# Optimization experiments

Measured on AMD Instinct MI355X. Metric: run time of the kernel, lower is better.

The kernel has to match this reference:

```python
import jax, jax.numpy as jnp
import numpy as np

N_NODES = 50000
N_EDGES = 600000
C = 128
T = 2          # layer index t
NU = 1         # DRew nu parameter
EPS = 0.0      # GIN eps


def mlp(x, W1, b1, W2, b2):
    # instantiate_mlp with final_activation=False, batch_norm=False:
    # Linear -> ReLU -> Linear
    return jax.nn.relu(x @ W1 + b1) @ W2 + b2


def setup_inputs() -> dict:
    key = jax.random.key(0)
    ks = jax.random.split(key, 16)
    node_embeddings = jax.random.normal(ks[0], (T + 1, N_NODES, C), dtype=jnp.float32)
    edge_index = jax.random.randint(ks[1], (2, N_EDGES), 0, N_NODES, dtype=jnp.int32)
    edge_weights = jax.random.randint(ks[2], (N_EDGES,), 1, T + 2, dtype=jnp.int32)  # hops 1..3
    s = 1.0 / np.sqrt(C)
    def lin(k):
        kw, kb = jax.random.split(k)
        return (jax.random.uniform(kw, (C, C), jnp.float32, -s, s),
                jax.random.uniform(kb, (C,), jnp.float32, -s, s))
    loop_W1, loop_b1 = lin(ks[3]); loop_W2, loop_b2 = lin(ks[4])
    rel_W1, rel_b1 = lin(ks[5]); rel_W2, rel_b2 = lin(ks[6])
    # T higher-hop MLPs (k = 2 .. T+1), stacked along axis 0
    hh1 = [lin(k) for k in jax.random.split(ks[7], T)]
    hh2 = [lin(k) for k in jax.random.split(ks[8], T)]
    hh_W1 = jnp.stack([w for w, _ in hh1]); hh_b1 = jnp.stack([b for _, b in hh1])
    hh_W2 = jnp.stack([w for w, _ in hh2]); hh_b2 = jnp.stack([b for _, b in hh2])
    hop_coef = jax.random.normal(ks[9], (T + 1,), dtype=jnp.float32)
    return dict(t=T, node_embeddings=node_embeddings, edge_index=edge_index,
                edge_weights=edge_weights,
                loop_W1=loop_W1, loop_b1=loop_b1, loop_W2=loop_W2, loop_b2=loop_b2,
                rel_W1=rel_W1, rel_b1=rel_b1, rel_W2=rel_W2, rel_b2=rel_b2,
                hh_W1=hh_W1, hh_b1=hh_b1, hh_W2=hh_W2, hh_b2=hh_b2,
                hop_coef=hop_coef)


def reference(t, node_embeddings, edge_index, edge_weights,
              loop_W1, loop_b1, loop_W2, loop_b2,
              rel_W1, rel_b1, rel_W2, rel_b2,
              hh_W1, hh_b1, hh_W2, hh_b2, hop_coef):
    x_t = node_embeddings[t]                       # [N, C]
    n = x_t.shape[0]
    row, col = edge_index[0], edge_index[1]        # sparse A: out[row] += X[col]
    dt = x_t.dtype

    hops = []
    # hop 1: relational MLP on current-layer embeddings
    h1 = mlp(x_t, rel_W1, rel_b1, rel_W2, rel_b2)
    m1 = (edge_weights == 1).astype(dt)[:, None]
    hops.append(jax.ops.segment_sum(h1[col] * m1, row, num_segments=n))
    # hops k = 2 .. t+1: per-hop MLP on delayed embeddings (DRew)
    for k in range(2, t + 2):
        delay = max(0, k - NU)
        hk = mlp(node_embeddings[t - delay],
                 hh_W1[k - 2], hh_b1[k - 2], hh_W2[k - 2], hh_b2[k - 2])
        mk = (edge_weights == k).astype(dt)[:, None]
        hops.append(jax.ops.segment_sum(hk[col] * mk, row, num_segments=n))

    by_hop = jnp.stack(hops)                       # [t+1, N, C]
    self_term = mlp((1.0 + EPS) * x_t, loop_W1, loop_b1, loop_W2, loop_b2)
    return self_term + jnp.einsum('k,knc->nc', hop_coef, by_hop)
```

## Files before the change

### kernel.cpp

```cpp
#include <hip/hip_runtime.h>

#define N_NODES 50000
#define N_EDGES 600000
#define C 128
#define STRIPS 3125
#define GROUPS 3125
#define N_TASKS 4

typedef __bf16 bf16;
typedef __attribute__((ext_vector_type(8))) __bf16 bf16x8;
typedef __attribute__((ext_vector_type(4))) __bf16 bf16x4;
typedef __attribute__((ext_vector_type(2))) __bf16 bf16x2;
typedef __attribute__((ext_vector_type(4))) float f32x4;
typedef __attribute__((ext_vector_type(2))) float f32x2;

struct PtrsV { const void* p[8]; };

__device__ __forceinline__ int bf16_wild(unsigned short w) {
    int exp = (w >> 7) & 0xFF;
    int mant = w & 0x7F;
    if (exp == 0xFF) return 1;
    if (exp >= 133) return 1;
    if (exp == 0) return mant != 0 ? 1 : 0;
    if (exp <= 114) return 1;
    return 0;
}

__global__ void __launch_bounds__(256) detect_zero_kernel(
    const unsigned short* __restrict__ emb,
    const unsigned short* __restrict__ w,
    const unsigned short* __restrict__ b,
    const unsigned short* __restrict__ hc,
    int* __restrict__ flags, int* __restrict__ deg)
{
    if (blockIdx.x == 0) {
        int lane = threadIdx.x;
        if (lane >= 64) return;
        int ce = 0, cw = 0, cb = 0, ch = 0;
        for (int j = 0; j < 4; ++j) {
            ce += bf16_wild(emb[lane * 4 + j]);
            cw += bf16_wild(w[lane * 4 + j]);
        }
        for (int j = 0; j < 2; ++j) cb += bf16_wild(b[lane * 2 + j]);
        if (lane < 3) ch = bf16_wild(hc[lane]);
        for (int off = 32; off > 0; off >>= 1) {
            ce += __shfl_down(ce, off);
            cw += __shfl_down(cw, off);
            cb += __shfl_down(cb, off);
            ch += __shfl_down(ch, off);
        }
        if (lane == 0) {
            int wf = (cw >= 16) ? 1 : 0;
            flags[0] = (ce >= 16) ? 1 : 0;
            flags[1] = wf;
            flags[2] = (cb >= 8) ? 1 : 0;
            flags[3] = (ch > 0) ? 1 : wf;
        }
    } else {
        int i = (blockIdx.x - 1) * 256 + threadIdx.x;
        if (i < N_NODES) deg[i] = 0;
    }
}

__global__ void __launch_bounds__(256) pack_kernel(
    PtrsV wmats, PtrsV bvecs, const void* hc_raw,
    const int* __restrict__ flags,
    bf16* __restrict__ pw, float* __restrict__ cbias, float* __restrict__ ccoef)
{
    int tid = blockIdx.x * 256 + threadIdx.x;
    int wf = flags[1], bfl = flags[2], hf = flags[3];
    if (tid < 8 * 16384) {
        int m    = tid >> 14;
        int r    = tid & 16383;
        int j    = r & 7;
        int lane = (r >> 3) & 63;
        int n0   = (r >> 9) & 7;
        int kk   = r >> 12;
        int k = kk * 32 + (lane >> 4) * 8 + j;
        int n = n0 * 16 + (lane & 15);
        int idx = k * C + n + ((m == 4 || m == 5) ? 16384 : 0);
        float v = wf ? ((const float*)wmats.p[m])[idx]
                     : (float)((const bf16*)wmats.p[m])[idx];
        pw[tid] = (bf16)v;
    } else if (tid < 8 * 16384 + 1024) {
        int j = tid - 8 * 16384;
        int m = j >> 7, n = j & 127;
        int idx = n + ((m == 4 || m == 5) ? 128 : 0);
        float v = bfl ? ((const float*)bvecs.p[m])[idx]
                      : (float)((const bf16*)bvecs.p[m])[idx];
        cbias[j] = v;
    } else if (tid < 8 * 16384 + 1024 + 3) {
        int i = tid - (8 * 16384 + 1024);
        float v = hf ? ((const float*)hc_raw)[i]
                     : (float)((const bf16*)hc_raw)[i];
        ccoef[i] = v;
    }
}

__global__ __launch_bounds__(256, 4) void mlp_kernel(
    const void* __restrict__ emb_raw,
    const bf16* __restrict__ pw,
    const float* __restrict__ cbias,
    const float* __restrict__ ccoef,
    const int* __restrict__ flags,
    bf16* __restrict__ h,
    bf16* __restrict__ hs)
{
    __shared__ bf16 sH[4][16][136];
    const int tid  = threadIdx.x;
    const int wave = tid >> 6, lane = tid & 63;
    const int wid  = blockIdx.x * 4 + wave;
    if (wid >= N_TASKS * GROUPS) return;
    const int task = wid & 3;
    const int grp  = wid >> 2;
    const int lrow = lane & 15, lquad = lane >> 4;
    bf16 (*sh)[136] = sH[wave];

    const int m1_of[4] = {0, 2, 4, 6};
    const int ly_of[4] = {2, 1, 0, 2};
    const int m1 = m1_of[task];
    const bf16x8* w1v = (const bf16x8*)(pw + (size_t)m1 * 16384);
    const bf16x8* w2v = w1v + 2048;
    const float oscale = (task == 0) ? ccoef[0] : (task == 1) ? ccoef[1]
                       : (task == 2) ? ccoef[2] : 1.0f;
    bf16* outp = (task == 3) ? hs : (h + (size_t)task * N_NODES * C);
    const int emb_f32 = flags[0];
    const size_t lbase = (size_t)ly_of[task] * N_NODES * C;

    const int s0 = grp;

    float b1f[8], b2f[8];
    #pragma unroll
    for (int n0 = 0; n0 < 8; ++n0) {
        b1f[n0] = cbias[m1 * 128 + n0 * 16 + lrow];
        b2f[n0] = cbias[(m1 + 1) * 128 + n0 * 16 + lrow];
    }

    bf16x8 af[4];
    {
        size_t xb = lbase + (size_t)(s0 * 16 + lrow) * C + lquad * 8;
        if (emb_f32) {
            const float* xf = (const float*)emb_raw + xb;
            #pragma unroll
            for (int kk = 0; kk < 4; ++kk) {
                f32x4 u0 = *(const f32x4*)(xf + kk * 32);
                f32x4 u1 = *(const f32x4*)(xf + kk * 32 + 4);
                bf16x8 v;
                v[0]=(bf16)u0[0]; v[1]=(bf16)u0[1]; v[2]=(bf16)u0[2]; v[3]=(bf16)u0[3];
                v[4]=(bf16)u1[0]; v[5]=(bf16)u1[1]; v[6]=(bf16)u1[2]; v[7]=(bf16)u1[3];
                af[kk] = v;
            }
        } else {
            const bf16* x16 = (const bf16*)emb_raw + xb;
            #pragma unroll
            for (int kk = 0; kk < 4; ++kk)
                af[kk] = *(const bf16x8*)(x16 + kk * 32);
        }
    }

    #pragma unroll
    for (int n0 = 0; n0 < 8; ++n0) {
        bf16x8 bv0 = w1v[0 * 512 + n0 * 64 + lane];
        bf16x8 bv1 = w1v[1 * 512 + n0 * 64 + lane];
        bf16x8 bv2 = w1v[2 * 512 + n0 * 64 + lane];
        bf16x8 bv3 = w1v[3 * 512 + n0 * 64 + lane];
        int n = n0 * 16 + lrow;
        float bias = b1f[n0];
        f32x4 a4 = {0.f, 0.f, 0.f, 0.f};
        a4 = __builtin_amdgcn_mfma_f32_16x16x32_bf16(af[0], bv0, a4, 0, 0, 0);
        a4 = __builtin_amdgcn_mfma_f32_16x16x32_bf16(af[1], bv1, a4, 0, 0, 0);
        a4 = __builtin_amdgcn_mfma_f32_16x16x32_bf16(af[2], bv2, a4, 0, 0, 0);
        a4 = __builtin_amdgcn_mfma_f32_16x16x32_bf16(af[3], bv3, a4, 0, 0, 0);
        #pragma unroll
        for (int r = 0; r < 4; ++r) {
            float v = a4[r] + bias;
            v = v > 0.f ? v : 0.f;
            sh[lquad * 4 + r][n] = (bf16)v;
        }
    }

    bf16x8 ah[4];
    #pragma unroll
    for (int kk = 0; kk < 4; ++kk)
        ah[kk] = *(const bf16x8*)(&sh[lrow][kk * 32 + lquad * 8]);

    #pragma unroll
    for (int n0 = 0; n0 < 8; ++n0) {
        bf16x8 bv0 = w2v[0 * 512 + n0 * 64 + lane];
        bf16x8 bv1 = w2v[1 * 512 + n0 * 64 + lane];
        bf16x8 bv2 = w2v[2 * 512 + n0 * 64 + lane];
        bf16x8 bv3 = w2v[3 * 512 + n0 * 64 + lane];
        int n = n0 * 16 + lrow;
        float bias = b2f[n0];
        f32x4 a4 = {0.f, 0.f, 0.f, 0.f};
        a4 = __builtin_amdgcn_mfma_f32_16x16x32_bf16(ah[0], bv0, a4, 0, 0, 0);
        a4 = __builtin_amdgcn_mfma_f32_16x16x32_bf16(ah[1], bv1, a4, 0, 0, 0);
        a4 = __builtin_amdgcn_mfma_f32_16x16x32_bf16(ah[2], bv2, a4, 0, 0, 0);
        a4 = __builtin_amdgcn_mfma_f32_16x16x32_bf16(ah[3], bv3, a4, 0, 0, 0);
        #pragma unroll
        for (int r = 0; r < 4; ++r)
            sh[lquad * 4 + r][n] = (bf16)((a4[r] + bias) * oscale);
    }

    {
        int row = lane >> 2;
        int cs  = (lane & 3) * 32;
        bf16* dst = outp + (size_t)(s0 * 16) * C;
        #pragma unroll
        for (int j = 0; j < 4; ++j) {
            bf16x8 v = *(const bf16x8*)(&sh[row][cs + j * 8]);
            *(bf16x8*)(dst + (size_t)row * C + cs + j * 8) = v;
        }
    }
}

__global__ void __launch_bounds__(256) hist_kernel(
    const int* __restrict__ erow, int* __restrict__ deg)
{
    int e = blockIdx.x * 256 + threadIdx.x;
    if (e >= N_EDGES) return;
    atomicAdd(&deg[erow[e]], 1);
}

__device__ __forceinline__ int wave_incl_scan(int v, int lane) {
    int x = v;
    #pragma unroll
    for (int d = 1; d < 64; d <<= 1) {
        int t = __shfl_up(x, d);
        if (lane >= d) x += t;
    }
    return x;
}

__global__ void __launch_bounds__(256) scanA_kernel(
    const int* __restrict__ deg, int* __restrict__ offsets, int* __restrict__ btot)
{
    __shared__ int swave[4];
    int b = blockIdx.x, tid = threadIdx.x;
    int i = b * 256 + tid;
    int lane = tid & 63, wv = tid >> 6;
    int v = (i < N_NODES) ? deg[i] : 0;
    int x = wave_incl_scan(v, lane);
    if (lane == 63) swave[wv] = x;
    __syncthreads();
    int w0 = swave[0], w1 = swave[1], w2 = swave[2], w3 = swave[3];
    int wp = (wv > 0 ? w0 : 0) + (wv > 1 ? w1 : 0) + (wv > 2 ? w2 : 0);
    if (i < N_NODES) offsets[i] = wp + x - v;
    if (tid == 0) btot[b] = w0 + w1 + w2 + w3;
}

__global__ void __launch_bounds__(256) scanB_kernel(
    const int* __restrict__ btot, int* __restrict__ bbase, int nblk)
{
    __shared__ int swave[4];
    int tid = threadIdx.x;
    int lane = tid & 63, wv = tid >> 6;
    int v = (tid < nblk) ? btot[tid] : 0;
    int x = wave_incl_scan(v, lane);
    if (lane == 63) swave[wv] = x;
    __syncthreads();
    int w0 = swave[0], w1 = swave[1], w2 = swave[2], w3 = swave[3];
    int wp = (wv > 0 ? w0 : 0) + (wv > 1 ? w1 : 0) + (wv > 2 ? w2 : 0);
    if (tid < nblk) bbase[tid] = wp + x - v;
}

__global__ void __launch_bounds__(256) scanC_kernel(
    const int* __restrict__ bbase, int* __restrict__ offsets, int* __restrict__ cursor)
{
    int i = blockIdx.x * 256 + threadIdx.x;
    if (i < N_NODES) {
        int o = offsets[i] + bbase[blockIdx.x];
        offsets[i] = o;
        cursor[i] = o;
    }
    if (i == 0) offsets[N_NODES] = N_EDGES;
}

__global__ void __launch_bounds__(256) fill_kernel(
    const int* __restrict__ erow, const int* __restrict__ ecol,
    const int* __restrict__ ew,
    int* __restrict__ cursor, int* __restrict__ edata)
{
    int e = blockIdx.x * 256 + threadIdx.x;
    if (e >= N_EDGES) return;
    int dst = erow[e];
    int pos = atomicAdd(&cursor[dst], 1);
    edata[pos] = (ecol[e] << 2) | (ew[e] - 1);
}

__global__ void __launch_bounds__(256) gather_kernel(
    const int* __restrict__ offsets, const int* __restrict__ edata,
    const bf16* __restrict__ h,
    const bf16* __restrict__ hs,
    void* __restrict__ out,
    const int* __restrict__ flags)
{
    const int node = blockIdx.x * 4 + (threadIdx.x >> 6);
    if (node >= N_NODES) return;
    const int lane = threadIdx.x & 63;
    const int c = lane * 2;

    bf16x2 sv = *(const bf16x2*)(hs + (size_t)node * C + c);
    float a0 = (float)sv[0], a1 = (float)sv[1];

    const int s = offsets[node], e = offsets[node + 1];
    for (int base = s; base < e; base += 64) {
        int idx = base + lane;
        int ed_i = (idx < e) ? edata[idx] : 0;
        int cnt = e - base; if (cnt > 64) cnt = 64;
        int j = 0;
        for (; j + 8 <= cnt; j += 8) {
            float t0 = 0.f, t1 = 0.f;
            #pragma unroll
            for (int u = 0; u < 8; ++u) {
                int ed = __shfl(ed_i, j + u);
                bf16x2 v = *(const bf16x2*)(h + (size_t)(ed & 3) * (N_NODES * C)
                                              + (size_t)(ed >> 2) * C + c);
                t0 += (float)v[0];
                t1 += (float)v[1];
            }
            a0 += t0; a1 += t1;
        }
        for (; j + 4 <= cnt; j += 4) {
            int e0 = __shfl(ed_i, j);
            int e1 = __shfl(ed_i, j + 1);
            int e2 = __shfl(ed_i, j + 2);
            int e3 = __shfl(ed_i, j + 3);
            bf16x2 v0 = *(const bf16x2*)(h + (size_t)(e0 & 3) * (N_NODES * C) + (size_t)(e0 >> 2) * C + c);
            bf16x2 v1 = *(const bf16x2*)(h + (size_t)(e1 & 3) * (N_NODES * C) + (size_t)(e1 >> 2) * C + c);
            bf16x2 v2 = *(const bf16x2*)(h + (size_t)(e2 & 3) * (N_NODES * C) + (size_t)(e2 >> 2) * C + c);
            bf16x2 v3 = *(const bf16x2*)(h + (size_t)(e3 & 3) * (N_NODES * C) + (size_t)(e3 >> 2) * C + c);
            a0 += (float)v0[0] + (float)v1[0] + (float)v2[0] + (float)v3[0];
            a1 += (float)v0[1] + (float)v1[1] + (float)v2[1] + (float)v3[1];
        }
        for (; j < cnt; ++j) {
            int ed = __shfl(ed_i, j);
            bf16x2 v = *(const bf16x2*)(h + (size_t)(ed & 3) * (N_NODES * C) + (size_t)(ed >> 2) * C + c);
            a0 += (float)v[0];
            a1 += (float)v[1];
        }
    }

    if (flags[0]) {
        f32x2 o; o[0] = a0; o[1] = a1;
        *(f32x2*)((float*)out + (size_t)node * C + c) = o;
    } else {
        bf16x2 o; o[0] = (bf16)a0; o[1] = (bf16)a1;
        *(bf16x2*)((bf16*)out + (size_t)node * C + c) = o;
    }
}

extern "C" void kernel_launch(void* const* d_in, const int* in_sizes, int n_in,
                              void* d_out, int out_size, void* d_ws, size_t ws_size,
                              hipStream_t stream) {
    const void* emb = d_in[1];
    const int*  ei  = (const int*)d_in[2];
    const int*  ew  = (const int*)d_in[3];

    const size_t H_BYTES  = (size_t)3 * N_NODES * C * sizeof(bf16);
    const size_t HS_BYTES = (size_t)N_NODES * C * sizeof(bf16);
    const size_t PW_BYTES = (size_t)8 * 16384 * sizeof(bf16);
    bf16*  h      = (bf16*)d_ws;
    bf16*  hs     = (bf16*)((char*)d_ws + H_BYTES);
    bf16*  pw     = (bf16*)((char*)d_ws + H_BYTES + HS_BYTES);
    float* cbias  = (float*)((char*)d_ws + H_BYTES + HS_BYTES + PW_BYTES);
    float* ccoef  = cbias + 1024;
    int*   flags  = (int*)(ccoef + 4);
    int*   deg    = flags + 16;
    int*   cursor = deg + N_NODES;
    int*   offsets= cursor + N_NODES;
    int*   btot   = offsets + N_NODES + 8;
    int*   bbase  = btot + 256;
    int*   edata  = bbase + 256;

    PtrsV wptr;
    wptr.p[0] = d_in[8];   wptr.p[1] = d_in[10];
    wptr.p[2] = d_in[12];  wptr.p[3] = d_in[14];
    wptr.p[4] = d_in[12];  wptr.p[5] = d_in[14];
    wptr.p[6] = d_in[4];   wptr.p[7] = d_in[6];
    PtrsV bptr;
    bptr.p[0] = d_in[9];   bptr.p[1] = d_in[11];
    bptr.p[2] = d_in[13];  bptr.p[3] = d_in[15];
    bptr.p[4] = d_in[13];  bptr.p[5] = d_in[15];
    bptr.p[6] = d_in[5];   bptr.p[7] = d_in[7];

    const int NBLK = (N_NODES + 255) / 256;

    detect_zero_kernel<<<1 + NBLK, 256, 0, stream>>>(
        (const unsigned short*)emb, (const unsigned short*)d_in[8],
        (const unsigned short*)d_in[9], (const unsigned short*)d_in[16],
        flags, deg);

    pack_kernel<<<517, 256, 0, stream>>>(wptr, bptr, d_in[16], flags, pw, cbias, ccoef);

    const int* erow = ei;
    const int* ecol = ei + N_EDGES;
    hist_kernel<<<(N_EDGES + 255) / 256, 256, 0, stream>>>(erow, deg);
    scanA_kernel<<<NBLK, 256, 0, stream>>>(deg, offsets, btot);
    scanB_kernel<<<1, 256, 0, stream>>>(btot, bbase, NBLK);
    scanC_kernel<<<NBLK, 256, 0, stream>>>(bbase, offsets, cursor);
    fill_kernel<<<(N_EDGES + 255) / 256, 256, 0, stream>>>(erow, ecol, ew, cursor, edata);

    mlp_kernel<<<(N_TASKS * GROUPS + 3) / 4, 256, 0, stream>>>(
        emb, pw, cbias, ccoef, flags, h, hs);

    gather_kernel<<<(N_NODES + 3) / 4, 256, 0, stream>>>(
        offsets, edata, h, hs, d_out, flags);
}
```

Before: 297.1 us.

## Make MLP kernel persistent with LDS-resident weights and prefetched input strips

The MLP kernel becomes persistent: 256 blocks of 512 threads, each block pinned to one task. Each block stages that task's two 128x128 bf16 weight matrices (64 KB) into LDS once, then its waves loop over 16-row strips with a stride of 512 strips. The next strip's input rows are prefetched into registers while the current strip is computed. This replaces the per-wave global/L2 weight reads and the launch of many tiny blocks, at the cost of LDS capacity and occupancy and only 256 blocks on the device.

```diff
diff --git a/kernel.cpp b/kernel.cpp
--- a/kernel.cpp
+++ b/kernel.cpp
@@ -4,8 +4,9 @@
 #define N_EDGES 600000
 #define C 128
 #define STRIPS 3125
-#define GROUPS 3125
 #define N_TASKS 4
+#define MLP_BLOCKS 256
+#define SLOT_STRIDE 512
 
 typedef __bf16 bf16;
 typedef __attribute__((ext_vector_type(8))) __bf16 bf16x8;
@@ -97,7 +98,7 @@
     }
 }
 
-__global__ __launch_bounds__(256, 4) void mlp_kernel(
+__global__ __launch_bounds__(512, 2) void mlp_kernel(
     const void* __restrict__ emb_raw,
     const bf16* __restrict__ pw,
     const float* __restrict__ cbias,
@@ -106,28 +107,34 @@
     bf16* __restrict__ h,
     bf16* __restrict__ hs)
 {
-    __shared__ bf16 sH[4][16][136];
+    __shared__ bf16 sW[32768];
+    __shared__ bf16 sH[8][16][136];
     const int tid  = threadIdx.x;
     const int wave = tid >> 6, lane = tid & 63;
-    const int wid  = blockIdx.x * 4 + wave;
-    if (wid >= N_TASKS * GROUPS) return;
-    const int task = wid & 3;
-    const int grp  = wid >> 2;
+    const int task  = blockIdx.x & 3;
+    const int bslot = blockIdx.x >> 2;
     const int lrow = lane & 15, lquad = lane >> 4;
     bf16 (*sh)[136] = sH[wave];
 
     const int m1_of[4] = {0, 2, 4, 6};
     const int ly_of[4] = {2, 1, 0, 2};
     const int m1 = m1_of[task];
-    const bf16x8* w1v = (const bf16x8*)(pw + (size_t)m1 * 16384);
-    const bf16x8* w2v = w1v + 2048;
     const float oscale = (task == 0) ? ccoef[0] : (task == 1) ? ccoef[1]
                        : (task == 2) ? ccoef[2] : 1.0f;
     bf16* outp = (task == 3) ? hs : (h + (size_t)task * N_NODES * C);
     const int emb_f32 = flags[0];
     const size_t lbase = (size_t)ly_of[task] * N_NODES * C;
 
-    const int s0 = grp;
+    {
+        const f32x4* src = (const f32x4*)(pw + (size_t)m1 * 16384);
+        f32x4* dst = (f32x4*)sW;
+        #pragma unroll
+        for (int i = 0; i < 8; ++i)
+            dst[i * 512 + tid] = src[i * 512 + tid];
+    }
+    __syncthreads();
+    const bf16x8* w1v = (const bf16x8*)sW;
+    const bf16x8* w2v = w1v + 2048;
 
     float b1f[8], b2f[8];
     #pragma unroll
@@ -136,81 +143,117 @@
         b2f[n0] = cbias[(m1 + 1) * 128 + n0 * 16 + lrow];
     }
 
-    bf16x8 af[4];
+    int s = bslot * 8 + wave;
+    f32x4 u[8]; bf16x8 araw[4];
+
     {
-        size_t xb = lbase + (size_t)(s0 * 16 + lrow) * C + lquad * 8;
+        size_t xb = lbase + (size_t)(s * 16 + lrow) * C + lquad * 8;
         if (emb_f32) {
             const float* xf = (const float*)emb_raw + xb;
             #pragma unroll
             for (int kk = 0; kk < 4; ++kk) {
-                f32x4 u0 = *(const f32x4*)(xf + kk * 32);
-                f32x4 u1 = *(const f32x4*)(xf + kk * 32 + 4);
+                u[kk * 2]     = *(const f32x4*)(xf + kk * 32);
+                u[kk * 2 + 1] = *(const f32x4*)(xf + kk * 32 + 4);
+            }
+        } else {
+            const bf16* x16 = (const bf16*)emb_raw + xb;
+            #pragma unroll
+            for (int kk = 0; kk < 4; ++kk)
+                araw[kk] = *(const bf16x8*)(x16 + kk * 32);
+        }
+    }
+
+    while (s < STRIPS) {
+        const int snext = s + SLOT_STRIDE;
+
+        bf16x8 af[4];
+        if (emb_f32) {
+            #pragma unroll
+            for (int kk = 0; kk < 4; ++kk) {
+                f32x4 u0 = u[kk * 2], u1 = u[kk * 2 + 1];
                 bf16x8 v;
                 v[0]=(bf16)u0[0]; v[1]=(bf16)u0[1]; v[2]=(bf16)u0[2]; v[3]=(bf16)u0[3];
                 v[4]=(bf16)u1[0]; v[5]=(bf16)u1[1]; v[6]=(bf16)u1[2]; v[7]=(bf16)u1[3];
                 af[kk] = v;
             }
         } else {
-            const bf16* x16 = (const bf16*)emb_raw + xb;
-            #pragma unroll
-            for (int kk = 0; kk < 4; ++kk)
-                af[kk] = *(const bf16x8*)(x16 + kk * 32);
-        }
-    }
-
-    #pragma unroll
-    for (int n0 = 0; n0 < 8; ++n0) {
-        bf16x8 bv0 = w1v[0 * 512 + n0 * 64 + lane];
-        bf16x8 bv1 = w1v[1 * 512 + n0 * 64 + lane];
-        bf16x8 bv2 = w1v[2 * 512 + n0 * 64 + lane];
-        bf16x8 bv3 = w1v[3 * 512 + n0 * 64 + lane];
-        int n = n0 * 16 + lrow;
-        float bias = b1f[n0];
-        f32x4 a4 = {0.f, 0.f, 0.f, 0.f};
-        a4 = __builtin_amdgcn_mfma_f32_16x16x32_bf16(af[0], bv0, a4, 0, 0, 0);
-        a4 = __builtin_amdgcn_mfma_f32_16x16x32_bf16(af[1], bv1, a4, 0, 0, 0);
-        a4 = __builtin_amdgcn_mfma_f32_16x16x32_bf16(af[2], bv2, a4, 0, 0, 0);
-        a4 = __builtin_amdgcn_mfma_f32_16x16x32_bf16(af[3], bv3, a4, 0, 0, 0);
+            #pragma unroll
+            for (int kk = 0; kk < 4; ++kk) af[kk] = araw[kk];
+        }
+
+        if (snext < STRIPS) {
+            size_t xb = lbase + (size_t)(snext * 16 + lrow) * C + lquad * 8;
+            if (emb_f32) {
+                const float* xf = (const float*)emb_raw + xb;
+                #pragma unroll
+                for (int kk = 0; kk < 4; ++kk) {
+                    u[kk * 2]     = *(const f32x4*)(xf + kk * 32);
+                    u[kk * 2 + 1] = *(const f32x4*)(xf + kk * 32 + 4);
+                }
+            } else {
+                const bf16* x16 = (const bf16*)emb_raw + xb;
+                #pragma unroll
+                for (int kk = 0; kk < 4; ++kk)
+                    araw[kk] = *(const bf16x8*)(x16 + kk * 32);
+            }
+        }
+
         #pragma unroll
-        for (int r = 0; r < 4; ++r) {
-            float v = a4[r] + bias;
-            v = v > 0.f ? v : 0.f;
-            sh[lquad * 4 + r][n] = (bf16)v;
-        }
-    }
-
-    bf16x8 ah[4];
-    #pragma unroll
-    for (int kk = 0; kk < 4; ++kk)
-        ah[kk] = *(const bf16x8*)(&sh[lrow][kk * 32 + lquad * 8]);
-
-    #pragma unroll
-    for (int n0 = 0; n0 < 8; ++n0) {
-        bf16x8 bv0 = w2v[0 * 512 + n0 * 64 + lane];
-        bf16x8 bv1 = w2v[1 * 512 + n0 * 64 + lane];
-        bf16x8 bv2 = w2v[2 * 512 + n0 * 64 + lane];
-        bf16x8 bv3 = w2v[3 * 512 + n0 * 64 + lane];
-        int n = n0 * 16 + lrow;
-        float bias = b2f[n0];
-        f32x4 a4 = {0.f, 0.f, 0.f, 0.f};
-        a4 = __builtin_amdgcn_mfma_f32_16x16x32_bf16(ah[0], bv0, a4, 0, 0, 0);
-        a4 = __builtin_amdgcn_mfma_f32_16x16x32_bf16(ah[1], bv1, a4, 0, 0, 0);
-        a4 = __builtin_amdgcn_mfma_f32_16x16x32_bf16(ah[2], bv2, a4, 0, 0, 0);
-        a4 = __builtin_amdgcn_mfma_f32_16x16x32_bf16(ah[3], bv3, a4, 0, 0, 0);
+        for (int n0 = 0; n0 < 8; ++n0) {
+            bf16x8 bv0 = w1v[0 * 512 + n0 * 64 + lane];
+            bf16x8 bv1 = w1v[1 * 512 + n0 * 64 + lane];
+            bf16x8 bv2 = w1v[2 * 512 + n0 * 64 + lane];
+            bf16x8 bv3 = w1v[3 * 512 + n0 * 64 + lane];
+            int n = n0 * 16 + lrow;
+            float bias = b1f[n0];
+            f32x4 a4 = {0.f, 0.f, 0.f, 0.f};
+            a4 = __builtin_amdgcn_mfma_f32_16x16x32_bf16(af[0], bv0, a4, 0, 0, 0);
+            a4 = __builtin_amdgcn_mfma_f32_16x16x32_bf16(af[1], bv1, a4, 0, 0, 0);
+            a4 = __builtin_amdgcn_mfma_f32_16x16x32_bf16(af[2], bv2, a4, 0, 0, 0);
+            a4 = __builtin_amdgcn_mfma_f32_16x16x32_bf16(af[3], bv3, a4, 0, 0, 0);
+            #pragma unroll
+            for (int r = 0; r < 4; ++r) {
+                float v = a4[r] + bias;
+                v = v > 0.f ? v : 0.f;
+                sh[lquad * 4 + r][n] = (bf16)v;
+            }
+        }
+
+        bf16x8 ah[4];
         #pragma unroll
-        for (int r = 0; r < 4; ++r)
-            sh[lquad * 4 + r][n] = (bf16)((a4[r] + bias) * oscale);
-    }
-
-    {
-        int row = lane >> 2;
-        int cs  = (lane & 3) * 32;
-        bf16* dst = outp + (size_t)(s0 * 16) * C;
+        for (int kk = 0; kk < 4; ++kk)
+            ah[kk] = *(const bf16x8*)(&sh[lrow][kk * 32 + lquad * 8]);
+
         #pragma unroll
-        for (int j = 0; j < 4; ++j) {
-            bf16x8 v = *(const bf16x8*)(&sh[row][cs + j * 8]);
-            *(bf16x8*)(dst + (size_t)row * C + cs + j * 8) = v;
-        }
+        for (int n0 = 0; n0 < 8; ++n0) {
+            bf16x8 bv0 = w2v[0 * 512 + n0 * 64 + lane];
+            bf16x8 bv1 = w2v[1 * 512 + n0 * 64 + lane];
+            bf16x8 bv2 = w2v[2 * 512 + n0 * 64 + lane];
+            bf16x8 bv3 = w2v[3 * 512 + n0 * 64 + lane];
+            int n = n0 * 16 + lrow;
+            float bias = b2f[n0];
+            f32x4 a4 = {0.f, 0.f, 0.f, 0.f};
+            a4 = __builtin_amdgcn_mfma_f32_16x16x32_bf16(ah[0], bv0, a4, 0, 0, 0);
+            a4 = __builtin_amdgcn_mfma_f32_16x16x32_bf16(ah[1], bv1, a4, 0, 0, 0);
+            a4 = __builtin_amdgcn_mfma_f32_16x16x32_bf16(ah[2], bv2, a4, 0, 0, 0);
+            a4 = __builtin_amdgcn_mfma_f32_16x16x32_bf16(ah[3], bv3, a4, 0, 0, 0);
+            #pragma unroll
+            for (int r = 0; r < 4; ++r)
+                sh[lquad * 4 + r][n] = (bf16)((a4[r] + bias) * oscale);
+        }
+
+        {
+            int row = lane >> 2;
+            int cs  = (lane & 3) * 32;
+            bf16* dst = outp + (size_t)(s * 16) * C;
+            #pragma unroll
+            for (int j = 0; j < 4; ++j) {
+                bf16x8 v = *(const bf16x8*)(&sh[row][cs + j * 8]);
+                *(bf16x8*)(dst + (size_t)row * C + cs + j * 8) = v;
+            }
+        }
+
+        s = snext;
     }
 }
 
@@ -401,7 +444,7 @@
     scanC_kernel<<<NBLK, 256, 0, stream>>>(bbase, offsets, cursor);
     fill_kernel<<<(N_EDGES + 255) / 256, 256, 0, stream>>>(erow, ecol, ew, cursor, edata);
 
-    mlp_kernel<<<(N_TASKS * GROUPS + 3) / 4, 256, 0, stream>>>(
+    mlp_kernel<<<MLP_BLOCKS, 512, 0, stream>>>(
         emb, pw, cbias, ccoef, flags, h, hs);
 
     gather_kernel<<<(N_NODES + 3) / 4, 256, 0, stream>>>(
```

Measured after the change: 269.4 us. 9.3% less time.
